# Kernel optimization log

Measured on AMD Instinct MI355X. Metric: run time of the kernel, lower is better.

## Reference

```python
import jax, jax.numpy as jnp
import numpy as np

N_NODES = 100000
N_EDGES = 3200000
N_GRAPHS = 3200

def setup_inputs() -> dict:
    key = jax.random.key(0)
    ks = jax.random.split(key, 12)
    def glorot(k, shape):
        lim = np.sqrt(6.0 / (shape[0] + shape[1]))
        return jax.random.uniform(k, shape, jnp.float32, -lim, lim)
    x = jax.random.normal(ks[0], (N_NODES, 37), jnp.float32)
    edge_index = jax.random.randint(ks[1], (2, N_EDGES), 0, N_NODES, jnp.int64 if jax.config.jax_enable_x64 else jnp.int32)
    batch = jnp.sort(jax.random.randint(ks[2], (N_NODES,), 0, N_GRAPHS))
    return {
        'x': x,
        'W1': glorot(ks[3], (37, 128)),  'b1': jnp.zeros((128,), jnp.float32),
        'W2': glorot(ks[4], (128, 256)), 'b2': jnp.zeros((256,), jnp.float32),
        'W3': glorot(ks[5], (256, 256)), 'b3': jnp.zeros((256,), jnp.float32),
        'Wp': glorot(ks[6], (256, 256)), 'bp': jnp.zeros((256,), jnp.float32),
        'edge_index': edge_index,
        'batch': batch,
    }

def _gcn_conv(h, W, b, src, dst, dis):
    # PyG GCNConv: h' = D^{-1/2}(A+I)D^{-1/2} (h W) + b, self-loops added
    hW = h @ W
    norm = dis[src] * dis[dst]                      # [E]
    msg = hW[src] * norm[:, None]                   # gather + scale
    agg = jax.ops.segment_sum(msg, dst, num_segments=N_NODES)
    agg = agg + hW * (dis * dis)[:, None]           # self-loop contribution
    return agg + b

def reference(x, W1, b1, W2, b2, W3, b3, Wp, bp, edge_index, batch):
    src, dst = edge_index[0], edge_index[1]
    # degree with self-loops (all edge weights = 1)
    deg = jax.ops.segment_sum(jnp.ones((N_EDGES,), x.dtype), dst, num_segments=N_NODES) + 1.0
    dis = jax.lax.rsqrt(deg)
    h = jax.nn.relu(_gcn_conv(x, W1, b1, src, dst, dis))
    h = jax.nn.relu(_gcn_conv(h, W2, b2, src, dst, dis))
    h = jax.nn.relu(_gcn_conv(h, W3, b3, src, dst, dis))
    # global mean pool over graphs
    sums = jax.ops.segment_sum(h, batch, num_segments=N_GRAPHS)
    cnts = jax.ops.segment_sum(jnp.ones((N_NODES,), x.dtype), batch, num_segments=N_GRAPHS)
    pooled = sums / jnp.maximum(cnts, 1.0)[:, None]
    return pooled @ Wp + bp
```

## Files before the change

kernel.cpp:

```cpp
#include <hip/hip_runtime.h>

#define N_NODES  100000
#define N_EDGES  3200000
#define N_GRAPHS 3200

#define NBLK 200
#define EB   16000
#define BSH  7
#define NB   ((N_NODES + 127) >> BSH)
#define BCAP 5120

typedef __attribute__((ext_vector_type(8))) short bf16x8;
typedef __attribute__((ext_vector_type(4))) float f32x4;

__device__ __forceinline__ float bf2f(unsigned short u) {
    return __uint_as_float(((unsigned)u) << 16);
}
__device__ __forceinline__ unsigned short f2bf(float f) {
    unsigned u = __float_as_uint(f);
    u += 0x7fffu + ((u >> 16) & 1u);
    return (unsigned short)(u >> 16);
}


__global__ __launch_bounds__(256, 4)
void hist_kernel(const int* __restrict__ dst, int* __restrict__ hist) {
    __shared__ int lh[NB];
    int blk = blockIdx.x, t = threadIdx.x;
    for (int b = t; b < NB; b += 256) lh[b] = 0;
    __syncthreads();
    int e0 = blk * EB;
    for (int i = t; i < EB; i += 256)
        atomicAdd(&lh[dst[e0 + i] >> BSH], 1);
    __syncthreads();
    for (int b = t; b < NB; b += 256) hist[b * NBLK + blk] = lh[b];
}

__global__ void bucket_tot_kernel(const int* __restrict__ hist, int* __restrict__ tot) {
    int b = blockIdx.x, l = threadIdx.x;
    int s = 0;
    for (int k = l; k < NBLK; k += 64) s += hist[b * NBLK + k];
    for (int off = 32; off; off >>= 1) s += __shfl_down(s, off);
    if (l == 0) tot[b] = s;
}

__global__ void bucket_scan_kernel(const int* __restrict__ tot, int* __restrict__ bucketStart) {
    __shared__ int part[256];
    int t = threadIdx.x;
    int chunk = (NB + 255) / 256;
    int lo = t * chunk; if (lo > NB) lo = NB;
    int hi = lo + chunk; if (hi > NB) hi = NB;
    int s = 0;
    for (int i = lo; i < hi; ++i) s += tot[i];
    part[t] = s;
    __syncthreads();
    for (int off = 1; off < 256; off <<= 1) {
        int v = part[t];
        int a = (t >= off) ? part[t - off] : 0;
        __syncthreads();
        part[t] = v + a;
        __syncthreads();
    }
    int run = (t == 0) ? 0 : part[t - 1];
    for (int i = lo; i < hi; ++i) { bucketStart[i] = run; run += tot[i]; }
    if (t == 255) bucketStart[NB] = run;
}

__global__ void bucket_base_kernel(int* __restrict__ hist, const int* __restrict__ bucketStart) {
    int b = blockIdx.x * blockDim.x + threadIdx.x;
    if (b >= NB) return;
    int run = bucketStart[b];
    int* row = hist + b * NBLK;
#pragma unroll 4
    for (int k = 0; k < NBLK; ++k) { int v = row[k]; row[k] = run; run += v; }
}

__global__ __launch_bounds__(256, 4)
void scatter1_kernel(const int* __restrict__ src, const int* __restrict__ dst,
                     const int* __restrict__ base,
                     int* __restrict__ sdst, int* __restrict__ ssrc) {
    __shared__ int lcur[NB];
    int blk = blockIdx.x, t = threadIdx.x;
    for (int b = t; b < NB; b += 256) lcur[b] = base[b * NBLK + blk];
    __syncthreads();
    int e0 = blk * EB;
    for (int i = t; i < EB; i += 256) {
        int d = dst[e0 + i], s = src[e0 + i];
        int pos = atomicAdd(&lcur[d >> BSH], 1);
        sdst[pos] = d;
        ssrc[pos] = s;
    }
}

__global__ __launch_bounds__(256, 1)
void csr2_kernel(const int* __restrict__ sdst, const int* __restrict__ ssrc,
                 const int* __restrict__ bucketStart,
                 int* __restrict__ offsets, float* __restrict__ dis,
                 int* __restrict__ csr_src) {
    __shared__ int ldst[BCAP];
    __shared__ int lsrc[BCAP];
    __shared__ int lhist[128], loff[128], lcur[128];
    int b = blockIdx.x, t = threadIdx.x;
    int n0 = b << BSH;
    int e0 = bucketStart[b], e1 = bucketStart[b + 1];
    int cnt = e1 - e0; if (cnt > BCAP) cnt = BCAP;
    for (int i = t; i < cnt; i += 256) {
        ldst[i] = sdst[e0 + i] - n0;
        lsrc[i] = ssrc[e0 + i];
    }
    if (t < 128) lhist[t] = 0;
    __syncthreads();
    for (int i = t; i < cnt; i += 256) atomicAdd(&lhist[ldst[i]], 1);
    __syncthreads();
    if (t < 128) loff[t] = lhist[t];
    __syncthreads();
    for (int off = 1; off < 128; off <<= 1) {
        int v = 0;
        if (t < 128) { v = loff[t]; if (t >= off) v += loff[t - off]; }
        __syncthreads();
        if (t < 128) loff[t] = v;
        __syncthreads();
    }
    if (t < 128) {
        int excl = loff[t] - lhist[t];
        lcur[t] = excl;
        int n = n0 + t;
        if (n < N_NODES) {
            offsets[n] = e0 + excl;
            dis[n] = rsqrtf((float)lhist[t] + 1.0f);
        }
    }
    if (b == 0 && t == 0) offsets[N_NODES] = N_EDGES;
    __syncthreads();
    for (int i = t; i < cnt; i += 256) {
        int pos = atomicAdd(&lcur[ldst[i]], 1);
        csr_src[e0 + pos] = lsrc[i];
    }
}

template<int K, int N>
__global__ void pack_w_kernel(const float* __restrict__ W, int Krows,
                              unsigned short* __restrict__ hi,
                              unsigned short* __restrict__ lo) {
    constexpr int KS = K / 32;
    int idx = blockIdx.x * blockDim.x + threadIdx.x;
    if (idx >= (N / 16) * KS * 64) return;
    int l = idx & 63;
    int s = (idx >> 6) % KS;
    int t = idx / (64 * KS);
    int k0 = s * 32 + (l >> 4) * 8;
    int n  = t * 16 + (l & 15);
    size_t base = (size_t)idx * 8;
#pragma unroll
    for (int j = 0; j < 8; ++j) {
        int k = k0 + j;
        float w = (k < Krows) ? W[(size_t)k * N + n] : 0.0f;
        unsigned short h = f2bf(w);
        float rem = w - bf2f(h);
        hi[base + j] = h;
        lo[base + j] = f2bf(rem);
    }
}

__global__ __launch_bounds__(256, 4)
void cast_x_kernel(const float* __restrict__ x, const float* __restrict__ dis,
                   unsigned short* __restrict__ xb) {
    int idx = blockIdx.x * blockDim.x + threadIdx.x;
    if (idx >= N_NODES * 64) return;
    int n = idx >> 6, c = idx & 63;
    xb[idx] = (c < 37) ? f2bf(x[(size_t)n * 37 + c] * dis[n]) : (unsigned short)0;
}

template<int F>
__device__ __forceinline__ void agg_range(const unsigned short* __restrict__ tab,
                                          const int* __restrict__ csr_src,
                                          int j, int hi, int lane, float* acc) {
    for (; j + 16 <= hi; j += 16) {
        int sidx[16];
#pragma unroll
        for (int u = 0; u < 16; ++u) sidx[u] = csr_src[j + u];
        if (F == 64) {
            unsigned short v[16];
#pragma unroll
            for (int u = 0; u < 16; ++u) v[u] = tab[(size_t)sidx[u] * 64 + lane];
#pragma unroll
            for (int u = 0; u < 16; ++u) acc[0] += bf2f(v[u]);
        } else if (F == 128) {
            ushort2 v[16];
#pragma unroll
            for (int u = 0; u < 16; ++u)
                v[u] = ((const ushort2*)(tab + (size_t)sidx[u] * F))[lane];
#pragma unroll
            for (int u = 0; u < 16; ++u) { acc[0] += bf2f(v[u].x); acc[1] += bf2f(v[u].y); }
        } else {
            ushort4 v[16];
#pragma unroll
            for (int u = 0; u < 16; ++u)
                v[u] = ((const ushort4*)(tab + (size_t)sidx[u] * F))[lane];
#pragma unroll
            for (int u = 0; u < 16; ++u) {
                acc[0] += bf2f(v[u].x); acc[1] += bf2f(v[u].y);
                acc[2] += bf2f(v[u].z); acc[3] += bf2f(v[u].w);
            }
        }
    }
    for (; j + 4 <= hi; j += 4) {
        int sidx[4];
#pragma unroll
        for (int u = 0; u < 4; ++u) sidx[u] = csr_src[j + u];
        if (F == 64) {
            unsigned short v[4];
#pragma unroll
            for (int u = 0; u < 4; ++u) v[u] = tab[(size_t)sidx[u] * 64 + lane];
#pragma unroll
            for (int u = 0; u < 4; ++u) acc[0] += bf2f(v[u]);
        } else if (F == 128) {
            ushort2 v[4];
#pragma unroll
            for (int u = 0; u < 4; ++u)
                v[u] = ((const ushort2*)(tab + (size_t)sidx[u] * F))[lane];
#pragma unroll
            for (int u = 0; u < 4; ++u) { acc[0] += bf2f(v[u].x); acc[1] += bf2f(v[u].y); }
        } else {
            ushort4 v[4];
#pragma unroll
            for (int u = 0; u < 4; ++u)
                v[u] = ((const ushort4*)(tab + (size_t)sidx[u] * F))[lane];
#pragma unroll
            for (int u = 0; u < 4; ++u) {
                acc[0] += bf2f(v[u].x); acc[1] += bf2f(v[u].y);
                acc[2] += bf2f(v[u].z); acc[3] += bf2f(v[u].w);
            }
        }
    }
    for (; j < hi; ++j) {
        int s = csr_src[j];
        if (F == 64) {
            acc[0] += bf2f(tab[(size_t)s * 64 + lane]);
        } else if (F == 128) {
            ushort2 u = ((const ushort2*)(tab + (size_t)s * F))[lane];
            acc[0] += bf2f(u.x); acc[1] += bf2f(u.y);
        } else {
            ushort4 u = ((const ushort4*)(tab + (size_t)s * F))[lane];
            acc[0] += bf2f(u.x); acc[1] += bf2f(u.y); acc[2] += bf2f(u.z); acc[3] += bf2f(u.w);
        }
    }
}

template<int K, int NTW, int N, int MODE>
__global__ __launch_bounds__(256, 4)
void fused_agg_gemm(const unsigned short* __restrict__ tab,
                    const int* __restrict__ csr_src,
                    const int* __restrict__ offsets,
                    const float* __restrict__ dis,
                    const unsigned short* __restrict__ Bhi,
                    const unsigned short* __restrict__ Blo,
                    const float* __restrict__ bias,
                    unsigned short* __restrict__ out) {
    constexpr int KS = K / 32;
    __shared__ unsigned short ldsA[32 * K];
    char* lb = (char*)ldsA;
    int l = threadIdx.x & 63;
    int w = threadIdx.x >> 6;
    int m0 = blockIdx.x * 32;

    for (int i = 0; i < 8; ++i) {
        int r = w * 8 + i;
        int n = m0 + r;
        float acc[(K + 63) / 64];
        if (K == 64) {
            acc[0] = bf2f(tab[(size_t)n * 64 + l]);
        } else if (K == 128) {
            ushort2 u = ((const ushort2*)(tab + (size_t)n * K))[l];
            acc[0] = bf2f(u.x); acc[1] = bf2f(u.y);
        } else {
            ushort4 u = ((const ushort4*)(tab + (size_t)n * K))[l];
            acc[0] = bf2f(u.x); acc[1] = bf2f(u.y); acc[2] = bf2f(u.z); acc[3] = bf2f(u.w);
        }
        agg_range<K>(tab, csr_src, offsets[n], offsets[n + 1], l, acc);
        float d = dis[n];
        unsigned sw = (unsigned)((r & 7) << 4);
        if (K == 64) {
            *(unsigned short*)(lb + ((unsigned)(r * 128 + l * 2) ^ sw)) = f2bf(d * acc[0]);
        } else if (K == 128) {
            ushort2 o; o.x = f2bf(d * acc[0]); o.y = f2bf(d * acc[1]);
            *(ushort2*)(lb + ((unsigned)(r * 256 + l * 4) ^ sw)) = o;
        } else {
            ushort4 o;
            o.x = f2bf(d * acc[0]); o.y = f2bf(d * acc[1]);
            o.z = f2bf(d * acc[2]); o.w = f2bf(d * acc[3]);
            *(ushort4*)(lb + ((unsigned)(r * 512 + l * 8) ^ sw)) = o;
        }
    }
    __syncthreads();

    int n0 = w * (NTW * 16);
    f32x4 acc0[NTW], acc1[NTW];
#pragma unroll
    for (int tn = 0; tn < NTW; ++tn) { acc0[tn] = (f32x4){0,0,0,0}; acc1[tn] = (f32x4){0,0,0,0}; }

    int r0 = l & 15, r1 = r0 + 16;
    unsigned sw0 = (unsigned)((r0 & 7) << 4);
#pragma unroll
    for (int s = 0; s < KS; ++s) {
        unsigned kb = (unsigned)(s * 64 + (l >> 4) * 16);
        bf16x8 af0 = *(const bf16x8*)(lb + ((unsigned)(r0 * K * 2 + kb) ^ sw0));
        bf16x8 af1 = *(const bf16x8*)(lb + ((unsigned)(r1 * K * 2 + kb) ^ sw0));
#pragma unroll
        for (int tn = 0; tn < NTW; ++tn) {
            int t = (n0 >> 4) + tn;
            size_t boff = ((size_t)(t * KS + s) * 64 + l) * 8;
            bf16x8 bh = *(const bf16x8*)(Bhi + boff);
            bf16x8 bl = *(const bf16x8*)(Blo + boff);
            acc0[tn] = __builtin_amdgcn_mfma_f32_16x16x32_bf16(af0, bh, acc0[tn], 0, 0, 0);
            acc0[tn] = __builtin_amdgcn_mfma_f32_16x16x32_bf16(af0, bl, acc0[tn], 0, 0, 0);
            acc1[tn] = __builtin_amdgcn_mfma_f32_16x16x32_bf16(af1, bh, acc1[tn], 0, 0, 0);
            acc1[tn] = __builtin_amdgcn_mfma_f32_16x16x32_bf16(af1, bl, acc1[tn], 0, 0, 0);
        }
    }

    int rowg = (l >> 4) * 4;
#pragma unroll
    for (int tn = 0; tn < NTW; ++tn) {
        int n = n0 + tn * 16 + (l & 15);
        float b = bias[n];
#pragma unroll
        for (int r = 0; r < 4; ++r) {
#pragma unroll
            for (int half = 0; half < 2; ++half) {
                int m = m0 + half * 16 + rowg + r;
                float v = fmaxf((half ? acc1[tn][r] : acc0[tn][r]) + b, 0.0f);
                if (MODE == 1) out[(size_t)m * N + n] = f2bf(v * dis[m]);
                else           out[(size_t)m * N + n] = f2bf(v);
            }
        }
    }
}

__device__ __forceinline__ int lower_bound_dev(const int* __restrict__ a, int n, int key) {
    int lo = 0, hi = n;
    while (lo < hi) {
        int mid = (lo + hi) >> 1;
        if (a[mid] < key) lo = mid + 1; else hi = mid;
    }
    return lo;
}

__global__ __launch_bounds__(256, 4)
void pool_bf16_kernel(const unsigned short* __restrict__ h, const int* __restrict__ batch,
                      float* __restrict__ pooled) {
    int wave = threadIdx.x >> 6;
    int lane = threadIdx.x & 63;
    int g = blockIdx.x * 4 + wave;
    int lo = lower_bound_dev(batch, N_NODES, g);
    int hi = lower_bound_dev(batch, N_NODES, g + 1);
    float a0 = 0, a1 = 0, a2 = 0, a3 = 0;
    for (int n = lo; n < hi; ++n) {
        ushort4 u = ((const ushort4*)(h + (size_t)n * 256))[lane];
        a0 += bf2f(u.x); a1 += bf2f(u.y); a2 += bf2f(u.z); a3 += bf2f(u.w);
    }
    float inv = 1.0f / fmaxf((float)(hi - lo), 1.0f);
    float4 o = {a0 * inv, a1 * inv, a2 * inv, a3 * inv};
    *(float4*)&pooled[(size_t)g * 256 + lane * 4] = o;
}

__global__ __launch_bounds__(256, 2)
void head_gemm_kernel(const float* __restrict__ H, const float* __restrict__ W,
                      const float* __restrict__ bias, float* __restrict__ out) {
    __shared__ float lds[16 * 256];
    int row0 = blockIdx.x * 16;
    int t = threadIdx.x;
    const float* src = H + (size_t)row0 * 256;
    for (int i = t; i < 16 * 256; i += 256) lds[i] = src[i];
    __syncthreads();
    float acc[16];
#pragma unroll
    for (int r = 0; r < 16; ++r) acc[r] = 0.0f;
#pragma unroll 4
    for (int k = 0; k < 256; ++k) {
        float wv = W[k * 256 + t];
#pragma unroll
        for (int r = 0; r < 16; ++r) acc[r] += lds[r * 256 + k] * wv;
    }
#pragma unroll
    for (int r = 0; r < 16; ++r)
        out[(size_t)(row0 + r) * 256 + t] = acc[r] + bias[t];
}

static inline size_t align_up(size_t x, size_t a) { return (x + a - 1) & ~(a - 1); }

extern "C" void kernel_launch(void* const* d_in, const int* in_sizes, int n_in,
                              void* d_out, int out_size, void* d_ws, size_t ws_size,
                              hipStream_t stream) {
    const float* x  = (const float*)d_in[0];
    const float* W1 = (const float*)d_in[1];
    const float* b1 = (const float*)d_in[2];
    const float* W2 = (const float*)d_in[3];
    const float* b2 = (const float*)d_in[4];
    const float* W3 = (const float*)d_in[5];
    const float* b3 = (const float*)d_in[6];
    const float* Wp = (const float*)d_in[7];
    const float* bp = (const float*)d_in[8];
    const int*   ei = (const int*)d_in[9];
    const int*   batch = (const int*)d_in[10];
    float* out = (float*)d_out;

    const int* e_src = ei;
    const int* e_dst = ei + N_EDGES;

    char* p = (char*)d_ws;
    size_t off = 0;
    auto take = [&](size_t bytes) {
        void* r = p + off;
        off = align_up(off + bytes, 256);
        return r;
    };
    int*   hist        = (int*)  take(sizeof(int) * NB * NBLK);
    int*   tot         = (int*)  take(sizeof(int) * NB);
    int*   bucketStart = (int*)  take(sizeof(int) * (NB + 1));
    int*   offsets     = (int*)  take(sizeof(int) * (N_NODES + 1));
    int*   csr_src     = (int*)  take(sizeof(int) * N_EDGES);
    float* dis         = (float*)take(sizeof(float) * N_NODES);
    float* pooled      = (float*)take(sizeof(float) * N_GRAPHS * 256);
    unsigned short* whi1 = (unsigned short*)take(sizeof(unsigned short) * 64 * 128);
    unsigned short* wlo1 = (unsigned short*)take(sizeof(unsigned short) * 64 * 128);
    unsigned short* whi2 = (unsigned short*)take(sizeof(unsigned short) * 128 * 256);
    unsigned short* wlo2 = (unsigned short*)take(sizeof(unsigned short) * 128 * 256);
    unsigned short* whi3 = (unsigned short*)take(sizeof(unsigned short) * 256 * 256);
    unsigned short* wlo3 = (unsigned short*)take(sizeof(unsigned short) * 256 * 256);
    unsigned short* bufX = (unsigned short*)take(sizeof(unsigned short) * (size_t)N_NODES * 256);
    unsigned short* bufY = (unsigned short*)take(sizeof(unsigned short) * (size_t)N_NODES * 256);
    unsigned short* h3   = (unsigned short*)take(sizeof(unsigned short) * (size_t)N_NODES * 256);

    int* sdst = (int*)h3;
    int* ssrc = sdst + N_EDGES;

    unsigned short* xb     = bufY;
    unsigned short* table2 = bufX;
    unsigned short* table3 = bufY;

    hist_kernel<<<NBLK, 256, 0, stream>>>(e_dst, hist);
    bucket_tot_kernel<<<NB, 64, 0, stream>>>(hist, tot);
    bucket_scan_kernel<<<1, 256, 0, stream>>>(tot, bucketStart);
    bucket_base_kernel<<<(NB + 255) / 256, 256, 0, stream>>>(hist, bucketStart);
    scatter1_kernel<<<NBLK, 256, 0, stream>>>(e_src, e_dst, hist, sdst, ssrc);
    csr2_kernel<<<NB, 256, 0, stream>>>(sdst, ssrc, bucketStart, offsets, dis, csr_src);

    pack_w_kernel<64, 128><<<((128 / 16) * 2 * 64 + 255) / 256, 256, 0, stream>>>(W1, 37, whi1, wlo1);
    pack_w_kernel<128, 256><<<((256 / 16) * 4 * 64 + 255) / 256, 256, 0, stream>>>(W2, 128, whi2, wlo2);
    pack_w_kernel<256, 256><<<((256 / 16) * 8 * 64 + 255) / 256, 256, 0, stream>>>(W3, 256, whi3, wlo3);

    cast_x_kernel<<<(N_NODES * 64 + 255) / 256, 256, 0, stream>>>(x, dis, xb);
    fused_agg_gemm<64, 2, 128, 1><<<N_NODES / 32, 256, 0, stream>>>(
        xb, csr_src, offsets, dis, whi1, wlo1, b1, table2);

    fused_agg_gemm<128, 4, 256, 1><<<N_NODES / 32, 256, 0, stream>>>(
        table2, csr_src, offsets, dis, whi2, wlo2, b2, table3);

    fused_agg_gemm<256, 4, 256, 2><<<N_NODES / 32, 256, 0, stream>>>(
        table3, csr_src, offsets, dis, whi3, wlo3, b3, h3);

    pool_bf16_kernel<<<N_GRAPHS / 4, 256, 0, stream>>>(h3, batch, pooled);
    head_gemm_kernel<<<N_GRAPHS / 16, 256, 0, stream>>>(pooled, Wp, bp, out);
}
```

Before: 661.8 us.

## Pack local dst and src into one int for bucket scatter; raise agg-gemm occupancy

The intermediate bucketed edge arrays become a single packed 32-bit word per edge: 7 bits for the destination offset within its bucket and 17 bits for the source. This halves the global writes in scatter1, the reads in csr2, and csr2's LDS footprint. Separately, fused_agg_gemm's launch bounds ask for 8 blocks per CU instead of 4, which may force register spills. The packing depends on node indices fitting in 17 bits, which holds for 100000 nodes.

```diff
diff --git a/kernel.cpp b/kernel.cpp
--- a/kernel.cpp
+++ b/kernel.cpp
@@ -77,8 +77,7 @@
 
 __global__ __launch_bounds__(256, 4)
 void scatter1_kernel(const int* __restrict__ src, const int* __restrict__ dst,
-                     const int* __restrict__ base,
-                     int* __restrict__ sdst, int* __restrict__ ssrc) {
+                     const int* __restrict__ base, int* __restrict__ spk) {
     __shared__ int lcur[NB];
     int blk = blockIdx.x, t = threadIdx.x;
     for (int b = t; b < NB; b += 256) lcur[b] = base[b * NBLK + blk];
@@ -87,30 +86,25 @@
     for (int i = t; i < EB; i += 256) {
         int d = dst[e0 + i], s = src[e0 + i];
         int pos = atomicAdd(&lcur[d >> BSH], 1);
-        sdst[pos] = d;
-        ssrc[pos] = s;
+        spk[pos] = ((d & 127) << 17) | s;
     }
 }
 
 __global__ __launch_bounds__(256, 1)
-void csr2_kernel(const int* __restrict__ sdst, const int* __restrict__ ssrc,
+void csr2_kernel(const int* __restrict__ spk,
                  const int* __restrict__ bucketStart,
                  int* __restrict__ offsets, float* __restrict__ dis,
                  int* __restrict__ csr_src) {
-    __shared__ int ldst[BCAP];
-    __shared__ int lsrc[BCAP];
+    __shared__ int lpk[BCAP];
     __shared__ int lhist[128], loff[128], lcur[128];
     int b = blockIdx.x, t = threadIdx.x;
     int n0 = b << BSH;
     int e0 = bucketStart[b], e1 = bucketStart[b + 1];
     int cnt = e1 - e0; if (cnt > BCAP) cnt = BCAP;
-    for (int i = t; i < cnt; i += 256) {
-        ldst[i] = sdst[e0 + i] - n0;
-        lsrc[i] = ssrc[e0 + i];
-    }
+    for (int i = t; i < cnt; i += 256) lpk[i] = spk[e0 + i];
     if (t < 128) lhist[t] = 0;
     __syncthreads();
-    for (int i = t; i < cnt; i += 256) atomicAdd(&lhist[ldst[i]], 1);
+    for (int i = t; i < cnt; i += 256) atomicAdd(&lhist[lpk[i] >> 17], 1);
     __syncthreads();
     if (t < 128) loff[t] = lhist[t];
     __syncthreads();
@@ -133,8 +127,9 @@
     if (b == 0 && t == 0) offsets[N_NODES] = N_EDGES;
     __syncthreads();
     for (int i = t; i < cnt; i += 256) {
-        int pos = atomicAdd(&lcur[ldst[i]], 1);
-        csr_src[e0 + pos] = lsrc[i];
+        int v = lpk[i];
+        int pos = atomicAdd(&lcur[v >> 17], 1);
+        csr_src[e0 + pos] = v & 0x1FFFF;
     }
 }
 
@@ -248,7 +243,7 @@
 }
 
 template<int K, int NTW, int N, int MODE>
-__global__ __launch_bounds__(256, 4)
+__global__ __launch_bounds__(256, 8)
 void fused_agg_gemm(const unsigned short* __restrict__ tab,
                     const int* __restrict__ csr_src,
                     const int* __restrict__ offsets,
@@ -432,8 +427,7 @@
     unsigned short* bufY = (unsigned short*)take(sizeof(unsigned short) * (size_t)N_NODES * 256);
     unsigned short* h3   = (unsigned short*)take(sizeof(unsigned short) * (size_t)N_NODES * 256);
 
-    int* sdst = (int*)h3;
-    int* ssrc = sdst + N_EDGES;
+    int* spk = (int*)h3;
 
     unsigned short* xb     = bufY;
     unsigned short* table2 = bufX;
@@ -443,8 +437,8 @@
     bucket_tot_kernel<<<NB, 64, 0, stream>>>(hist, tot);
     bucket_scan_kernel<<<1, 256, 0, stream>>>(tot, bucketStart);
     bucket_base_kernel<<<(NB + 255) / 256, 256, 0, stream>>>(hist, bucketStart);
-    scatter1_kernel<<<NBLK, 256, 0, stream>>>(e_src, e_dst, hist, sdst, ssrc);
-    csr2_kernel<<<NB, 256, 0, stream>>>(sdst, ssrc, bucketStart, offsets, dis, csr_src);
+    scatter1_kernel<<<NBLK, 256, 0, stream>>>(e_src, e_dst, hist, spk);
+    csr2_kernel<<<NB, 256, 0, stream>>>(spk, bucketStart, offsets, dis, csr_src);
 
     pack_w_kernel<64, 128><<<((128 / 16) * 2 * 64 + 255) / 256, 256, 0, stream>>>(W1, 37, whi1, wlo1);
     pack_w_kernel<128, 256><<<((256 / 16) * 4 * 64 + 255) / 256, 256, 0, stream>>>(W2, 128, whi2, wlo2);
```

Result: faster. 625.1 us, median of 2 (-5.6%).
